# Performance work log

Hardware: AMD Instinct MI355X
Metric: run time of the kernel (lower is better)

Reference implementation:

```python
import jax, jax.numpy as jnp
import numpy as np

N = 50000
E = 600000
D_IN = 128
D_HID = 128
D_OUT = 40
EPS = 1e-5


def glorot(key, shape):
    lim = float(np.sqrt(6.0 / (shape[0] + shape[1])))
    return jax.random.uniform(key, shape, jnp.float32, -lim, lim)


def setup_inputs() -> dict:
    key = jax.random.key(0)
    ks = jax.random.split(key, 8)
    return {
        "node_feat": jax.random.normal(ks[0], (N, D_IN), jnp.float32),
        "edge_src": jax.random.randint(ks[1], (E,), 0, N, jnp.int32),
        "edge_dst": jax.random.randint(ks[2], (E,), 0, N, jnp.int32),
        # input BatchNorm (bn_1)
        "bn0_g": jnp.ones((D_IN,), jnp.float32),
        "bn0_b": jnp.zeros((D_IN,), jnp.float32),
        # conv 1 (in -> hidden) + its BN
        "W1": glorot(ks[3], (D_IN, D_HID)),
        "b1": jnp.zeros((D_HID,), jnp.float32),
        "bn1_g": jnp.ones((D_HID,), jnp.float32),
        "bn1_b": jnp.zeros((D_HID,), jnp.float32),
        # conv 2 (hidden -> hidden) + its BN
        "W2": glorot(ks[4], (D_HID, D_HID)),
        "b2": jnp.zeros((D_HID,), jnp.float32),
        "bn2_g": jnp.ones((D_HID,), jnp.float32),
        "bn2_b": jnp.zeros((D_HID,), jnp.float32),
        # final projection
        "Wf": glorot(ks[5], (D_HID, D_OUT)),
        "bf": jnp.zeros((D_OUT,), jnp.float32),
    }


def batchnorm(x, gamma, beta):
    # BatchNorm1d over nodes (batch-stat / training-mode normalization)
    mu = jnp.mean(x, axis=0)
    var = jnp.mean(jnp.square(x - mu), axis=0)
    return gamma * (x - mu) * jax.lax.rsqrt(var + EPS) + beta


def gcn_conv(x, W, b, src, dst, norm, self_norm):
    # GCNConv: D^{-1/2}(A+I)D^{-1/2} X W + b
    h = x @ W  # [N, d_out]
    agg = jax.ops.segment_sum(h[src] * norm[:, None], dst, num_segments=N)
    agg = agg + h * self_norm[:, None]  # self-loop contribution
    return agg + b


def reference(node_feat, edge_src, edge_dst, bn0_g, bn0_b, W1, b1, bn1_g, bn1_b,
              W2, b2, bn2_g, bn2_b, Wf, bf):
    # degree with self-loops: deg_i = |{e : dst(e)=i}| + 1
    deg = jnp.ones((N,), jnp.float32).at[edge_dst].add(1.0)
    dinv = jax.lax.rsqrt(deg)
    norm = dinv[edge_src] * dinv[edge_dst]  # [E]
    self_norm = dinv * dinv                 # [N]

    x = batchnorm(node_feat, bn0_g, bn0_b)

    x = gcn_conv(x, W1, b1, edge_src, edge_dst, norm, self_norm)
    x = batchnorm(x, bn1_g, bn1_b)
    x = jax.nn.relu(x)  # dropout is identity in eval mode

    x = gcn_conv(x, W2, b2, edge_src, edge_dst, norm, self_norm)
    x = batchnorm(x, bn2_g, bn2_b)
    x = jax.nn.relu(x)

    return x @ Wf + bf  # [N, D_OUT]
```

## Files before the change

kernel.cpp:

```cpp
#include <hip/hip_runtime.h>
#include <cstdint>
#include <cstddef>


#define CS_BLOCKS  512
#define AGG_BLOCKS 2048

typedef short s8v __attribute__((ext_vector_type(8)));
typedef float f4v __attribute__((ext_vector_type(4)));

__device__ inline ushort f2bf(float f) {
    uint u = __float_as_uint(f);
    return (ushort)((u + 0x7fffu + ((u >> 16) & 1u)) >> 16);
}
__device__ inline float2 bf2f2(uint u) {
    float2 r;
    r.x = __uint_as_float(u << 16);
    r.y = __uint_as_float(u & 0xffff0000u);
    return r;
}

__global__ __launch_bounds__(256) void k_colstats(const float* __restrict__ X,
                                                  int n,
                                                  float* __restrict__ part) {
    __shared__ float ls[8 * 128];
    __shared__ float lq[8 * 128];
    const int c4    = threadIdx.x & 31;
    const int rslot = threadIdx.x >> 5;
    float4 s4 = make_float4(0.f, 0.f, 0.f, 0.f);
    float4 q4 = make_float4(0.f, 0.f, 0.f, 0.f);
    const float4* X4 = (const float4*)X;
    for (int r = blockIdx.x * 8 + rslot; r < n; r += CS_BLOCKS * 8) {
        float4 v = X4[(size_t)r * 32 + c4];
        s4.x += v.x; s4.y += v.y; s4.z += v.z; s4.w += v.w;
        q4.x = fmaf(v.x, v.x, q4.x); q4.y = fmaf(v.y, v.y, q4.y);
        q4.z = fmaf(v.z, v.z, q4.z); q4.w = fmaf(v.w, v.w, q4.w);
    }
    *(float4*)&ls[rslot * 128 + c4 * 4] = s4;
    *(float4*)&lq[rslot * 128 + c4 * 4] = q4;
    __syncthreads();
    float t = 0.f;
    if (threadIdx.x < 128) {
        int c = threadIdx.x;
        #pragma unroll
        for (int k = 0; k < 8; ++k) t += ls[k * 128 + c];
    } else {
        int c = threadIdx.x - 128;
        #pragma unroll
        for (int k = 0; k < 8; ++k) t += lq[k * 128 + c];
    }
    part[blockIdx.x * 256 + threadIdx.x] = t;
}

__global__ __launch_bounds__(256) void k_redA(const float* __restrict__ part,
                                              float* __restrict__ part2) {
    const int c = threadIdx.x;
    const int b = blockIdx.x;
    float t = 0.f;
    #pragma unroll 4
    for (int j = 0; j < AGG_BLOCKS / 64; ++j)
        t += part[(size_t)(b * (AGG_BLOCKS / 64) + j) * 256 + c];
    part2[b * 256 + c] = t;
}

__global__ __launch_bounds__(1024) void k_bnfinal(const float* __restrict__ part,
                                                  int nrows,
                                                  const float* __restrict__ g,
                                                  const float* __restrict__ be,
                                                  float invn,
                                                  float* __restrict__ a,
                                                  float* __restrict__ b) {
    __shared__ float sh[4][256];
    const int c = threadIdx.x & 255;
    const int q = threadIdx.x >> 8;
    const int per = nrows >> 2;
    float t = 0.f;
    for (int r = q * per; r < q * per + per; r += 4) {
        t += part[(r + 0) * 256 + c] + part[(r + 1) * 256 + c]
           + part[(r + 2) * 256 + c] + part[(r + 3) * 256 + c];
    }
    sh[q][c] = t;
    __syncthreads();
    if (threadIdx.x < 128) {
        int cc = threadIdx.x;
        float su = sh[0][cc] + sh[1][cc] + sh[2][cc] + sh[3][cc];
        float sq = sh[0][cc + 128] + sh[1][cc + 128]
                 + sh[2][cc + 128] + sh[3][cc + 128];
        float mu  = su * invn;
        float var = sq * invn - mu * mu;
        float av  = g[cc] * rsqrtf(var + 1e-5f);
        a[cc] = av;
        b[cc] = be[cc] - mu * av;
    }
}

__global__ __launch_bounds__(256) void k_count(const int* __restrict__ dst, int e,
                                               int* __restrict__ cnt) {
    int i = blockIdx.x * 256 + threadIdx.x;
    if (i < e) atomicAdd(&cnt[dst[i]], 1);
}

__global__ __launch_bounds__(1024) void k_scanA(const int* __restrict__ cnt, int n,
                                                int* __restrict__ rs, int* __restrict__ bsum) {
    __shared__ int tmp[1024];
    int t = threadIdx.x;
    int i = blockIdx.x * 1024 + t;
    int v = (i < n) ? cnt[i] : 0;
    tmp[t] = v;
    __syncthreads();
    for (int off = 1; off < 1024; off <<= 1) {
        int x = (t >= off) ? tmp[t - off] : 0;
        __syncthreads();
        tmp[t] += x;
        __syncthreads();
    }
    if (i < n) rs[i] = tmp[t] - v;
    if (t == 1023) bsum[blockIdx.x] = tmp[t];
}

__global__ __launch_bounds__(256) void k_scanC(int* __restrict__ rs,
                                               const int* __restrict__ bsum,
                                               const int* __restrict__ cnt,
                                               float* __restrict__ dinv,
                                               int n, int e) {
    __shared__ int base;
    int chunk = (int)(blockIdx.x >> 2);
    if (threadIdx.x == 0) {
        int s = 0;
        for (int c = 0; c < chunk; ++c) s += bsum[c];
        base = s;
    }
    __syncthreads();
    int i = blockIdx.x * 256 + threadIdx.x;
    if (i < n) {
        rs[i] += base;
        dinv[i] = rsqrtf((float)(cnt[i] + 1));
    }
    if (blockIdx.x == 0 && threadIdx.x == 0) rs[n] = e;
}

__global__ __launch_bounds__(256) void k_fill(const int* __restrict__ src,
                                              const int* __restrict__ dst, int e,
                                              const int* __restrict__ rs,
                                              int* __restrict__ cursor,
                                              const float* __restrict__ dinv,
                                              int2* __restrict__ ep) {
    int i = blockIdx.x * 256 + threadIdx.x;
    if (i < e) {
        int d = dst[i], s = src[i];
        int p = rs[d] + atomicAdd(&cursor[d], 1);
        float nm = dinv[s] * dinv[d];
        ep[p] = make_int2(s, __float_as_int(nm));
    }
}

__global__ __launch_bounds__(256) void k_prep_w(const float* __restrict__ W,
                                                ushort* __restrict__ Wswz) {
    int t  = blockIdx.x * 256 + threadIdx.x;
    int l  = t & 63;
    int fi = t >> 6;
    int ks = fi & 3, ct = fi >> 2;
    int c  = ct * 16 + (l & 15);
    int k0 = ks * 32 + ((l >> 4) << 3);
    ushort o[8];
    #pragma unroll
    for (int j = 0; j < 8; ++j)
        o[j] = f2bf(W[(size_t)(k0 + j) * 128 + c]);
    ushort4* dst = (ushort4*)(Wswz + (size_t)t * 8);
    dst[0] = make_ushort4(o[0], o[1], o[2], o[3]);
    dst[1] = make_ushort4(o[4], o[5], o[6], o[7]);
}

__global__ __launch_bounds__(256) void k_gemm_mfma(const float* __restrict__ X,
                                                   const ushort* __restrict__ Wswz,
                                                   const float* __restrict__ av,
                                                   const float* __restrict__ bv,
                                                   int relu,
                                                   ushort* __restrict__ H, int n) {
    __shared__ ushort xb[64 * 128];
    const int tid  = threadIdx.x;
    const int row0 = blockIdx.x * 64;

    for (int i = tid; i < 64 * 32; i += 256) {
        int r = i >> 5, c4 = i & 31;
        int gr = row0 + r;
        float4 v = make_float4(0.f, 0.f, 0.f, 0.f);
        if (gr < n) v = ((const float4*)X)[(size_t)gr * 32 + c4];
        float4 a4 = ((const float4*)av)[c4];
        float4 b4 = ((const float4*)bv)[c4];
        v.x = fmaf(v.x, a4.x, b4.x);
        v.y = fmaf(v.y, a4.y, b4.y);
        v.z = fmaf(v.z, a4.z, b4.z);
        v.w = fmaf(v.w, a4.w, b4.w);
        if (relu) {
            v.x = fmaxf(v.x, 0.f); v.y = fmaxf(v.y, 0.f);
            v.z = fmaxf(v.z, 0.f); v.w = fmaxf(v.w, 0.f);
        }
        ushort4 pk = make_ushort4(f2bf(v.x), f2bf(v.y), f2bf(v.z), f2bf(v.w));
        int off = (r * 256 + c4 * 8) ^ ((r & 7) << 4);
        *(ushort4*)((char*)xb + off) = pk;
    }
    __syncthreads();

    const int wv = tid >> 6;
    const int l  = tid & 63;
    const int arow = wv * 16 + (l & 15);

    s8v afr[4];
    #pragma unroll
    for (int ks = 0; ks < 4; ++ks) {
        int off = (arow * 256 + ks * 64 + ((l >> 4) << 4)) ^ ((arow & 7) << 4);
        afr[ks] = *(const s8v*)((const char*)xb + off);
    }

    const s8v* wf = (const s8v*)Wswz;
    f4v acc[8];
    #pragma unroll
    for (int ct = 0; ct < 8; ++ct) {
        f4v c = {0.f, 0.f, 0.f, 0.f};
        #pragma unroll
        for (int ks = 0; ks < 4; ++ks) {
            s8v bb = wf[(ct * 4 + ks) * 64 + l];
            c = __builtin_amdgcn_mfma_f32_16x16x32_bf16(afr[ks], bb, c, 0, 0, 0);
        }
        acc[ct] = c;
    }

    const int rbase = row0 + wv * 16 + ((l >> 4) << 2);
    const int cidx  = l & 15;
    #pragma unroll
    for (int r = 0; r < 4; ++r) {
        int gr = rbase + r;
        if (gr < n) {
            #pragma unroll
            for (int ct = 0; ct < 8; ++ct)
                H[(size_t)gr * 128 + ct * 16 + cidx] = f2bf(acc[ct][r]);
        }
    }
}

__global__ __launch_bounds__(256) void k_aggregate(const ushort* __restrict__ H,
                                                   const int* __restrict__ rs,
                                                   const int2* __restrict__ ep,
                                                   const float* __restrict__ dinv,
                                                   float* __restrict__ AGG,
                                                   float* __restrict__ part, int n) {
    __shared__ float red[4][128];
    __shared__ float redq[4][128];
    const int wv   = threadIdx.x >> 6;
    const int lane = threadIdx.x & 63;
    float sx = 0.f, sy = 0.f, qx = 0.f, qy = 0.f;

    for (int node = blockIdx.x * 4 + wv; node < n; node += AGG_BLOCKS * 4) {
        float sn = dinv[node]; sn *= sn;
        float2 self = bf2f2(((const uint*)(H + (size_t)node * 128))[lane]);
        float2 acc;
        acc.x = self.x * sn; acc.y = self.y * sn;
        int i  = rs[node];
        int i1 = rs[node + 1];
        for (; i + 16 <= i1; i += 16) {
            int2 p[16];
            uint v[16];
            #pragma unroll
            for (int k = 0; k < 16; ++k) p[k] = ep[i + k];
            #pragma unroll
            for (int k = 0; k < 16; ++k)
                v[k] = ((const uint*)(H + (size_t)p[k].x * 128))[lane];
            #pragma unroll
            for (int k = 0; k < 16; ++k) {
                float w = __int_as_float(p[k].y);
                float2 f = bf2f2(v[k]);
                acc.x = fmaf(w, f.x, acc.x);
                acc.y = fmaf(w, f.y, acc.y);
            }
        }
        if (i + 8 <= i1) {
            int2 p[8];
            uint v[8];
            #pragma unroll
            for (int k = 0; k < 8; ++k) p[k] = ep[i + k];
            #pragma unroll
            for (int k = 0; k < 8; ++k)
                v[k] = ((const uint*)(H + (size_t)p[k].x * 128))[lane];
            #pragma unroll
            for (int k = 0; k < 8; ++k) {
                float w = __int_as_float(p[k].y);
                float2 f = bf2f2(v[k]);
                acc.x = fmaf(w, f.x, acc.x);
                acc.y = fmaf(w, f.y, acc.y);
            }
            i += 8;
        }
        if (i + 4 <= i1) {
            int2 p[4];
            uint v[4];
            #pragma unroll
            for (int k = 0; k < 4; ++k) p[k] = ep[i + k];
            #pragma unroll
            for (int k = 0; k < 4; ++k)
                v[k] = ((const uint*)(H + (size_t)p[k].x * 128))[lane];
            #pragma unroll
            for (int k = 0; k < 4; ++k) {
                float w = __int_as_float(p[k].y);
                float2 f = bf2f2(v[k]);
                acc.x = fmaf(w, f.x, acc.x);
                acc.y = fmaf(w, f.y, acc.y);
            }
            i += 4;
        }
        for (; i < i1; ++i) {
            int2 p = ep[i];
            float w = __int_as_float(p.y);
            float2 f = bf2f2(((const uint*)(H + (size_t)p.x * 128))[lane]);
            acc.x = fmaf(w, f.x, acc.x);
            acc.y = fmaf(w, f.y, acc.y);
        }
        ((float2*)(AGG + (size_t)node * 128))[lane] = acc;
        sx += acc.x; sy += acc.y;
        qx = fmaf(acc.x, acc.x, qx);
        qy = fmaf(acc.y, acc.y, qy);
    }

    red[wv][2 * lane]      = sx;
    red[wv][2 * lane + 1]  = sy;
    redq[wv][2 * lane]     = qx;
    redq[wv][2 * lane + 1] = qy;
    __syncthreads();
    const int t = threadIdx.x;
    if (t < 128)
        part[(size_t)blockIdx.x * 256 + t] =
            red[0][t] + red[1][t] + red[2][t] + red[3][t];
    else {
        int c = t - 128;
        part[(size_t)blockIdx.x * 256 + t] =
            redq[0][c] + redq[1][c] + redq[2][c] + redq[3][c];
    }
}

__global__ __launch_bounds__(256) void k_gemm_out(const float* __restrict__ X,
                                                  const float* __restrict__ Wf,
                                                  const float* __restrict__ bfv,
                                                  const float* __restrict__ a,
                                                  const float* __restrict__ b,
                                                  float* __restrict__ OUT, int n) {
    __shared__ float xl[32 * 132];
    __shared__ float wt[40 * 132];
    const int tid = threadIdx.x;

    for (int i = tid; i < 128 * 40; i += 256) {
        int c = i / 40;
        int j = i - c * 40;
        wt[j * 132 + c] = Wf[i];
    }
    const int row0 = blockIdx.x * 32;
    for (int i = tid; i < 32 * 32; i += 256) {
        int r = i >> 5, c4 = i & 31;
        int gr = row0 + r;
        float4 v = make_float4(0.f, 0.f, 0.f, 0.f);
        if (gr < n) v = ((const float4*)X)[(size_t)gr * 32 + c4];
        float4 a4 = ((const float4*)a)[c4];
        float4 b4 = ((const float4*)b)[c4];
        v.x = fmaxf(fmaf(v.x, a4.x, b4.x), 0.f);
        v.y = fmaxf(fmaf(v.y, a4.y, b4.y), 0.f);
        v.z = fmaxf(fmaf(v.z, a4.z, b4.z), 0.f);
        v.w = fmaxf(fmaf(v.w, a4.w, b4.w), 0.f);
        *(float4*)&xl[r * 132 + (c4 << 2)] = v;
    }
    __syncthreads();

    const int rg = tid >> 3;
    const int cg = tid & 7;
    const int j0 = cg * 5;
    float acc[5] = {0.f, 0.f, 0.f, 0.f, 0.f};
    for (int c = 0; c < 128; c += 4) {
        float4 xv = *(const float4*)&xl[rg * 132 + c];
        #pragma unroll
        for (int j = 0; j < 5; ++j) {
            float4 wv = *(const float4*)&wt[(j0 + j) * 132 + c];
            acc[j] = fmaf(xv.x, wv.x, acc[j]);
            acc[j] = fmaf(xv.y, wv.y, acc[j]);
            acc[j] = fmaf(xv.z, wv.z, acc[j]);
            acc[j] = fmaf(xv.w, wv.w, acc[j]);
        }
    }
    int gr = row0 + rg;
    if (gr < n) {
        #pragma unroll
        for (int j = 0; j < 5; ++j)
            OUT[(size_t)gr * 40 + j0 + j] = acc[j] + bfv[j0 + j];
    }
}

extern "C" void kernel_launch(void* const* d_in, const int* in_sizes, int n_in,
                              void* d_out, int out_size, void* d_ws, size_t ws_size,
                              hipStream_t stream) {
    const float* X0      = (const float*)d_in[0];
    const int*   edgesrc = (const int*)d_in[1];
    const int*   edgedst = (const int*)d_in[2];
    const float* bn0g = (const float*)d_in[3];
    const float* bn0b = (const float*)d_in[4];
    const float* W1   = (const float*)d_in[5];
    const float* bn1g = (const float*)d_in[7];
    const float* bn1b = (const float*)d_in[8];
    const float* W2   = (const float*)d_in[9];
    const float* bn2g = (const float*)d_in[11];
    const float* bn2b = (const float*)d_in[12];
    const float* Wf   = (const float*)d_in[13];
    const float* bfv  = (const float*)d_in[14];

    const int n = in_sizes[0] / 128;
    const int e = in_sizes[1];
    float* OUT = (float*)d_out;

    ushort* H    = (ushort*)d_ws;
    float*  AGG  = (float*)(H + (size_t)n * 128);
    float*  dinv = AGG + (size_t)n * 128;
    int2*   ep   = (int2*)(dinv + n);
    ushort* Wswz = (ushort*)(ep + e);
    int*    cnt  = (int*)(Wswz + 2 * 16384);
    int*    rs   = cnt + n;
    int*  cursor = rs + n + 1;
    int*    bsum = cursor + n;
    float*  part = (float*)(bsum + 64);
    float* part2 = part + (size_t)AGG_BLOCKS * 256;
    float* a0 = part2 + 64 * 256;       float* b0 = a0 + 128;
    float* a1 = b0 + 128;               float* b1 = a1 + 128;
    float* a2 = b1 + 128;               float* b2 = a2 + 128;

    hipMemsetAsync(cnt,    0, (size_t)n * sizeof(int), stream);
    hipMemsetAsync(cursor, 0, (size_t)n * sizeof(int), stream);

    const float invn = 1.f / (float)n;
    const int nb = (n + 1023) / 1024;

    k_prep_w<<<8, 256, 0, stream>>>(W1, Wswz);
    k_prep_w<<<8, 256, 0, stream>>>(W2, Wswz + 16384);

    k_count<<<(e + 255) / 256, 256, 0, stream>>>(edgedst, e, cnt);
    k_scanA<<<nb, 1024, 0, stream>>>(cnt, n, rs, bsum);
    k_scanC<<<(n + 255) / 256, 256, 0, stream>>>(rs, bsum, cnt, dinv, n, e);
    k_fill<<<(e + 255) / 256, 256, 0, stream>>>(edgesrc, edgedst, e, rs, cursor,
                                                dinv, ep);

    const int gemmBlocks = (n + 63) / 64;

    k_colstats<<<CS_BLOCKS, 256, 0, stream>>>(X0, n, part);
    k_bnfinal<<<1, 1024, 0, stream>>>(part, CS_BLOCKS, bn0g, bn0b, invn, a0, b0);
    k_gemm_mfma<<<gemmBlocks, 256, 0, stream>>>(X0, Wswz, a0, b0, 0, H, n);
    k_aggregate<<<AGG_BLOCKS, 256, 0, stream>>>(H, rs, ep, dinv, AGG, part, n);

    k_redA<<<64, 256, 0, stream>>>(part, part2);
    k_bnfinal<<<1, 1024, 0, stream>>>(part2, 64, bn1g, bn1b, invn, a1, b1);
    k_gemm_mfma<<<gemmBlocks, 256, 0, stream>>>(AGG, Wswz + 16384, a1, b1, 1, H, n);
    k_aggregate<<<AGG_BLOCKS, 256, 0, stream>>>(H, rs, ep, dinv, AGG, part, n);

    k_redA<<<64, 256, 0, stream>>>(part, part2);
    k_bnfinal<<<1, 1024, 0, stream>>>(part2, 64, bn2g, bn2b, invn, a2, b2);
    k_gemm_out<<<(n + 31) / 32, 256, 0, stream>>>(AGG, Wf, bfv, a2, b2, OUT, n);
}
```

Baseline: 246.7 us.

## Reuse count atomics for CSR fill and launch one aggregate wave per node

The degree-count kernel now stores each edge's atomic return as its rank within the destination row, so the fill kernel computes positions without a second atomic and the cursor memset is dropped. The aggregation kernel switches from a fixed grid-stride loop to one wave per node with a much larger grid, aiming for better load balance and latency hiding. In exchange, per-block partial stats grow to one row per block, which increases the reduction traffic in the follow-up kernel and the workspace size.

Result: slower. 256.8 us (+4.1%).

```diff
diff --git a/kernel.cpp b/kernel.cpp
--- a/kernel.cpp
+++ b/kernel.cpp
@@ -3,8 +3,7 @@
 #include <cstddef>
 
 
-#define CS_BLOCKS  512
-#define AGG_BLOCKS 2048
+#define CS_BLOCKS 512
 
 typedef short s8v __attribute__((ext_vector_type(8)));
 typedef float f4v __attribute__((ext_vector_type(4)));
@@ -53,14 +52,21 @@
 }
 
 __global__ __launch_bounds__(256) void k_redA(const float* __restrict__ part,
-                                              float* __restrict__ part2) {
+                                              float* __restrict__ part2,
+                                              int nrows) {
     const int c = threadIdx.x;
     const int b = blockIdx.x;
-    float t = 0.f;
-    #pragma unroll 4
-    for (int j = 0; j < AGG_BLOCKS / 64; ++j)
-        t += part[(size_t)(b * (AGG_BLOCKS / 64) + j) * 256 + c];
-    part2[b * 256 + c] = t;
+    const int per = (nrows + 63) >> 6;
+    const int r0 = b * per;
+    const int r1 = min(r0 + per, nrows);
+    float t0 = 0.f, t1 = 0.f;
+    int r = r0;
+    for (; r + 2 <= r1; r += 2) {
+        t0 += part[(size_t)r * 256 + c];
+        t1 += part[(size_t)(r + 1) * 256 + c];
+    }
+    if (r < r1) t0 += part[(size_t)r * 256 + c];
+    part2[b * 256 + c] = t0 + t1;
 }
 
 __global__ __launch_bounds__(1024) void k_bnfinal(const float* __restrict__ part,
@@ -95,9 +101,10 @@
 }
 
 __global__ __launch_bounds__(256) void k_count(const int* __restrict__ dst, int e,
-                                               int* __restrict__ cnt) {
+                                               int* __restrict__ cnt,
+                                               int* __restrict__ rank) {
     int i = blockIdx.x * 256 + threadIdx.x;
-    if (i < e) atomicAdd(&cnt[dst[i]], 1);
+    if (i < e) rank[i] = atomicAdd(&cnt[dst[i]], 1);
 }
 
 __global__ __launch_bounds__(1024) void k_scanA(const int* __restrict__ cnt, int n,
@@ -142,13 +149,13 @@
 __global__ __launch_bounds__(256) void k_fill(const int* __restrict__ src,
                                               const int* __restrict__ dst, int e,
                                               const int* __restrict__ rs,
-                                              int* __restrict__ cursor,
+                                              const int* __restrict__ rank,
                                               const float* __restrict__ dinv,
                                               int2* __restrict__ ep) {
     int i = blockIdx.x * 256 + threadIdx.x;
     if (i < e) {
         int d = dst[i], s = src[i];
-        int p = rs[d] + atomicAdd(&cursor[d], 1);
+        int p = rs[d] + rank[i];
         float nm = dinv[s] * dinv[d];
         ep[p] = make_int2(s, __float_as_int(nm));
     }
@@ -249,9 +256,10 @@
     __shared__ float redq[4][128];
     const int wv   = threadIdx.x >> 6;
     const int lane = threadIdx.x & 63;
+    const int node = blockIdx.x * 4 + wv;
     float sx = 0.f, sy = 0.f, qx = 0.f, qy = 0.f;
 
-    for (int node = blockIdx.x * 4 + wv; node < n; node += AGG_BLOCKS * 4) {
+    if (node < n) {
         float sn = dinv[node]; sn *= sn;
         float2 self = bf2f2(((const uint*)(H + (size_t)node * 128))[lane]);
         float2 acc;
@@ -316,9 +324,9 @@
             acc.y = fmaf(w, f.y, acc.y);
         }
         ((float2*)(AGG + (size_t)node * 128))[lane] = acc;
-        sx += acc.x; sy += acc.y;
-        qx = fmaf(acc.x, acc.x, qx);
-        qy = fmaf(acc.y, acc.y, qy);
+        sx = acc.x; sy = acc.y;
+        qx = acc.x * acc.x;
+        qy = acc.y * acc.y;
     }
 
     red[wv][2 * lane]      = sx;
@@ -412,6 +420,8 @@
     const int e = in_sizes[1];
     float* OUT = (float*)d_out;
 
+    const int aggBlocks = (n + 3) / 4;
+
     ushort* H    = (ushort*)d_ws;
     float*  AGG  = (float*)(H + (size_t)n * 128);
     float*  dinv = AGG + (size_t)n * 128;
@@ -419,16 +429,15 @@
     ushort* Wswz = (ushort*)(ep + e);
     int*    cnt  = (int*)(Wswz + 2 * 16384);
     int*    rs   = cnt + n;
-    int*  cursor = rs + n + 1;
-    int*    bsum = cursor + n;
+    int*    rank = rs + n + 1;
+    int*    bsum = rank + e;
     float*  part = (float*)(bsum + 64);
-    float* part2 = part + (size_t)AGG_BLOCKS * 256;
+    float* part2 = part + (size_t)aggBlocks * 256;
     float* a0 = part2 + 64 * 256;       float* b0 = a0 + 128;
     float* a1 = b0 + 128;               float* b1 = a1 + 128;
     float* a2 = b1 + 128;               float* b2 = a2 + 128;
 
-    hipMemsetAsync(cnt,    0, (size_t)n * sizeof(int), stream);
-    hipMemsetAsync(cursor, 0, (size_t)n * sizeof(int), stream);
+    hipMemsetAsync(cnt, 0, (size_t)n * sizeof(int), stream);
 
     const float invn = 1.f / (float)n;
     const int nb = (n + 1023) / 1024;
@@ -436,10 +445,10 @@
     k_prep_w<<<8, 256, 0, stream>>>(W1, Wswz);
     k_prep_w<<<8, 256, 0, stream>>>(W2, Wswz + 16384);
 
-    k_count<<<(e + 255) / 256, 256, 0, stream>>>(edgedst, e, cnt);
+    k_count<<<(e + 255) / 256, 256, 0, stream>>>(edgedst, e, cnt, rank);
     k_scanA<<<nb, 1024, 0, stream>>>(cnt, n, rs, bsum);
     k_scanC<<<(n + 255) / 256, 256, 0, stream>>>(rs, bsum, cnt, dinv, n, e);
-    k_fill<<<(e + 255) / 256, 256, 0, stream>>>(edgesrc, edgedst, e, rs, cursor,
+    k_fill<<<(e + 255) / 256, 256, 0, stream>>>(edgesrc, edgedst, e, rs, rank,
                                                 dinv, ep);
 
     const int gemmBlocks = (n + 63) / 64;
@@ -447,14 +456,14 @@
     k_colstats<<<CS_BLOCKS, 256, 0, stream>>>(X0, n, part);
     k_bnfinal<<<1, 1024, 0, stream>>>(part, CS_BLOCKS, bn0g, bn0b, invn, a0, b0);
     k_gemm_mfma<<<gemmBlocks, 256, 0, stream>>>(X0, Wswz, a0, b0, 0, H, n);
-    k_aggregate<<<AGG_BLOCKS, 256, 0, stream>>>(H, rs, ep, dinv, AGG, part, n);
-
-    k_redA<<<64, 256, 0, stream>>>(part, part2);
+    k_aggregate<<<aggBlocks, 256, 0, stream>>>(H, rs, ep, dinv, AGG, part, n);
+
+    k_redA<<<64, 256, 0, stream>>>(part, part2, aggBlocks);
     k_bnfinal<<<1, 1024, 0, stream>>>(part2, 64, bn1g, bn1b, invn, a1, b1);
     k_gemm_mfma<<<gemmBlocks, 256, 0, stream>>>(AGG, Wswz + 16384, a1, b1, 1, H, n);
-    k_aggregate<<<AGG_BLOCKS, 256, 0, stream>>>(H, rs, ep, dinv, AGG, part, n);
-
-    k_redA<<<64, 256, 0, stream>>>(part, part2);
+    k_aggregate<<<aggBlocks, 256, 0, stream>>>(H, rs, ep, dinv, AGG, part, n);
+
+    k_redA<<<64, 256, 0, stream>>>(part, part2, aggBlocks);
     k_bnfinal<<<1, 1024, 0, stream>>>(part2, 64, bn2g, bn2b, invn, a2, b2);
     k_gemm_out<<<(n + 31) / 32, 256, 0, stream>>>(AGG, Wf, bfv, a2, b2, OUT, n);
 }
```
